# Kernel tuning notes

Measured on AMD Instinct MI355X. Metric: run time of the kernel, lower is better.

The kernel has to match this reference:

```python
import jax, jax.numpy as jnp
import numpy as np

DIM = 256
HEADS = 8
DHEAD = 32
HIDDEN = HEADS * DHEAD
EPS = 1e-5


def layer_norm(x, g, b):
    mu = jnp.mean(x, axis=-1, keepdims=True)
    var = jnp.var(x, axis=-1, keepdims=True)
    return (x - mu) * jax.lax.rsqrt(var + EPS) * g + b


def rope(x):
    # x: [b, m, h, n, d]; interleaved-pair rotary embedding over axis n (lucidrains style)
    n, d = x.shape[-2], x.shape[-1]
    inv_freq = 1.0 / (10000.0 ** (jnp.arange(0, d, 2, dtype=jnp.float32) / d))  # [d/2]
    ang = jnp.arange(n, dtype=jnp.float32)[:, None] * inv_freq[None, :]         # [n, d/2]
    ang = jnp.repeat(ang, 2, axis=-1)                                           # [n, d]
    cos, sin = jnp.cos(ang), jnp.sin(ang)
    xp = x.reshape(x.shape[:-1] + (d // 2, 2))
    rot = jnp.stack((-xp[..., 1], xp[..., 0]), axis=-1).reshape(x.shape)
    return x * cos + rot * sin


def split_heads(t):
    b, m, n, _ = t.shape
    return t.reshape(b, m, n, HEADS, DHEAD).transpose(0, 1, 3, 2, 4)  # b m h n d


def temporal_attention(x, ctx, pos_bias, Wq, Wk, Wv, Wo):
    # x, ctx: [b, m, t, c] (already normalized)
    q = split_heads(x @ Wq) * (DHEAD ** -0.5)
    k = split_heads(ctx @ Wk)
    v = split_heads(ctx @ Wv)
    q, k = rope(q), rope(k)
    sim = jnp.einsum('bmhid,bmhjd->bmhij', q, k) + pos_bias[None]  # pos_bias [1,h,t,t]
    attn = jax.nn.softmax(sim, axis=-1)
    out = jnp.einsum('bmhij,bmhjd->bmhid', attn, v)
    b, m = out.shape[0], out.shape[1]
    out = out.transpose(0, 1, 3, 2, 4).reshape(b, m, -1, HIDDEN)
    return out @ Wo


def setup_inputs() -> dict:
    key = jax.random.key(0)
    ks = jax.random.split(key, 16)
    b, c, t, h, w = 2, DIM, 16, 32, 32
    s = 0.02
    inp = {
        'x': jax.random.normal(ks[0], (b, c, t, h, w), jnp.float32),
        'motion_map': jax.random.normal(ks[1], (b, c, t, h, w), jnp.float32),
        'pos_bias': jax.random.normal(ks[2], (1, HEADS, t, t), jnp.float32),
        'g1': jnp.ones((DIM,), jnp.float32), 'b1': jnp.zeros((DIM,), jnp.float32),
        'Wq1': jax.random.normal(ks[3], (DIM, HIDDEN), jnp.float32) * s,
        'Wk1': jax.random.normal(ks[4], (DIM, HIDDEN), jnp.float32) * s,
        'Wv1': jax.random.normal(ks[5], (DIM, HIDDEN), jnp.float32) * s,
        'Wo1': jax.random.normal(ks[6], (HIDDEN, DIM), jnp.float32) * s,
        'g2': jnp.ones((DIM,), jnp.float32), 'b2': jnp.zeros((DIM,), jnp.float32),
        'cg': jnp.ones((DIM,), jnp.float32), 'cb': jnp.zeros((DIM,), jnp.float32),
        'Wq2': jax.random.normal(ks[7], (DIM, HIDDEN), jnp.float32) * s,
        'Wk2': jax.random.normal(ks[8], (DIM, HIDDEN), jnp.float32) * s,
        'Wv2': jax.random.normal(ks[9], (DIM, HIDDEN), jnp.float32) * s,
        'Wo2': jax.random.normal(ks[10], (HIDDEN, DIM), jnp.float32) * s,
    }
    return inp


def reference(x, motion_map, pos_bias, g1, b1, Wq1, Wk1, Wv1, Wo1,
              g2, b2, cg, cb, Wq2, Wk2, Wv2, Wo2):
    b, c, t, h, w = x.shape
    xs = x.transpose(0, 3, 4, 2, 1).reshape(b, h * w, t, c)           # b (hw) t c
    mm = motion_map.transpose(0, 3, 4, 2, 1).reshape(b, h * w, t, c)
    # self attention
    xn = layer_norm(xs, g1, b1)
    xs = xs + temporal_attention(xn, xn, pos_bias, Wq1, Wk1, Wv1, Wo1)
    # cross attention with motion map
    xn2 = layer_norm(xs, g2, b2)
    ctx = layer_norm(mm, cg, cb)
    xs = xs + temporal_attention(xn2, ctx, pos_bias, Wq2, Wk2, Wv2, Wo2)
    return xs.reshape(b, h, w, t, c).transpose(0, 4, 3, 1, 2)          # b c t h w
```

## Files before the change

kernel.cpp:

```cpp
#include <hip/hip_runtime.h>

typedef __attribute__((ext_vector_type(4))) float f32x4;
typedef __attribute__((ext_vector_type(8))) short s16x8;

__device__ __forceinline__ unsigned short f2bf(float f) {
  union { float f; unsigned int i; } x; x.f = f;
  unsigned int lsb = (x.i >> 16) & 1u;
  x.i += 0x7fffu + lsb;
  return (unsigned short)(x.i >> 16);
}

__device__ __forceinline__ float bf2f(unsigned short u) {
  union { unsigned int i; float f; } x;
  x.i = ((unsigned int)u) << 16;
  return x.f;
}

__device__ __forceinline__ void gload_lds16(const void* gsrc, void* ldst) {
  __builtin_amdgcn_global_load_lds(
      (const __attribute__((address_space(1))) void*)gsrc,
      (__attribute__((address_space(3))) void*)ldst, 16, 0, 0);
}

__global__ void prep_w(const float* __restrict__ Wq1, const float* __restrict__ Wk1,
                       const float* __restrict__ Wv1, const float* __restrict__ Wo1,
                       const float* __restrict__ Wq2, const float* __restrict__ Wk2,
                       const float* __restrict__ Wv2, const float* __restrict__ Wo2,
                       unsigned short* __restrict__ W1t, unsigned short* __restrict__ Wo1t,
                       unsigned short* __restrict__ W2t, unsigned short* __restrict__ Wo2t,
                       float* __restrict__ ropeC, float* __restrict__ ropeS) {
  int blk = blockIdx.x, tid = threadIdx.x;
  if (blk < 768) {
    int n = blk, k = tid;
    const float* src = (n < 256) ? Wq1 : (n < 512 ? Wk1 : Wv1);
    W1t[n * 256 + k] = f2bf(src[k * 256 + (n & 255)]);
  } else if (blk < 1024) {
    int n = blk - 768, k = tid;
    Wo1t[n * 256 + k] = f2bf(Wo1[k * 256 + n]);
  } else if (blk < 1792) {
    int n = blk - 1024, k = tid;
    const float* src = (n < 256) ? Wq2 : (n < 512 ? Wk2 : Wv2);
    W2t[n * 256 + k] = f2bf(src[k * 256 + (n & 255)]);
  } else if (blk < 2048) {
    int n = blk - 1792, k = tid;
    Wo2t[n * 256 + k] = f2bf(Wo2[k * 256 + n]);
  } else {
    #pragma unroll
    for (int it = 0; it < 2; ++it) {
      int idx = it * 256 + tid;
      int t = idx >> 5, d = idx & 31;
      float inv = exp2f(-13.287712379549449f * (float)(d & 30) * (1.0f / 32.0f));
      float ang = (float)t * inv;
      ropeC[idx] = cosf(ang);
      ropeS[idx] = sinf(ang);
    }
  }
}

__global__ __launch_bounds__(256) void transpose_in(
    const float* __restrict__ X, const float* __restrict__ MM,
    void* __restrict__ xtv, void* __restrict__ mmtv, int outBf) {
  __shared__ float lds[32][257];
  int blk = blockIdx.x, tid = threadIdx.x;
  bool isX = blk < 1024;
  int idx = blk & 1023;
  int b = idx >> 9, t = (idx >> 5) & 15, h = idx & 31;
  const float* src = isX ? X : MM;

  int w_ = tid & 31, cg8 = tid >> 5;
  size_t base = (size_t)b * 4194304 + (size_t)t * 1024 + (size_t)h * 32 + w_;
  #pragma unroll
  for (int itr = 0; itr < 32; ++itr) {
    int c = itr * 8 + cg8;
    lds[w_][c] = src[base + (size_t)c * 16384];
  }
  __syncthreads();
  size_t seqb = ((size_t)b * 1024 + (size_t)h * 32) * 16 + t;
  if (outBf) {
    unsigned short* dstp = (unsigned short*)(isX ? xtv : mmtv);
    #pragma unroll
    for (int w2 = 0; w2 < 32; ++w2)
      dstp[(seqb + (size_t)w2 * 16) * 256 + tid] = f2bf(lds[w2][tid]);
  } else {
    float* dstp = (float*)(isX ? xtv : mmtv);
    #pragma unroll
    for (int w2 = 0; w2 < 32; ++w2)
      dstp[(seqb + (size_t)w2 * 16) * 256 + tid] = lds[w2][tid];
  }
}

__global__ __launch_bounds__(256) void ln_rows(
    const void* __restrict__ srcv, const float* __restrict__ gw,
    const float* __restrict__ bw, unsigned short* __restrict__ dst, int srcF32) {
  int tid = threadIdx.x;
  size_t row = (size_t)blockIdx.x * 16 + (tid >> 4);
  int l16 = tid & 15;
  float v[16], s = 0.f, q = 0.f;
  if (srcF32) {
    const float* sp = (const float*)srcv + row * 256 + l16 * 16;
    #pragma unroll
    for (int e = 0; e < 16; ++e) { v[e] = sp[e]; s += v[e]; q += v[e] * v[e]; }
  } else {
    const unsigned short* sp = (const unsigned short*)srcv + row * 256 + l16 * 16;
    #pragma unroll
    for (int e = 0; e < 16; ++e) { v[e] = bf2f(sp[e]); s += v[e]; q += v[e] * v[e]; }
  }
  s += __shfl_xor(s, 1); q += __shfl_xor(q, 1);
  s += __shfl_xor(s, 2); q += __shfl_xor(q, 2);
  s += __shfl_xor(s, 4); q += __shfl_xor(q, 4);
  s += __shfl_xor(s, 8); q += __shfl_xor(q, 8);
  float mu = s * (1.f / 256.f);
  float var = q * (1.f / 256.f) - mu * mu;
  float rs = rsqrtf(fmaxf(var, 0.f) + 1e-5f);
  #pragma unroll
  for (int e = 0; e < 16; ++e) {
    int c = l16 * 16 + e;
    dst[row * 256 + c] = f2bf((v[e] - mu) * rs * gw[c] + bw[c]);
  }
}

__device__ __forceinline__ void stage_tile(const unsigned short* __restrict__ src,
                                           size_t row0, unsigned short* lds,
                                           int k0, int tid) {
  #pragma unroll
  for (int it = 0; it < 2; ++it) {
    int o = (it * 256 + tid) * 16;
    int row = o >> 6;
    int ks = ((o >> 4) & 3) ^ ((row >> 1) & 3);
    gload_lds16(src + (row0 + (size_t)row) * 256 + k0 + ks * 8, (char*)lds + o);
  }
}

__device__ __forceinline__ s16x8 frag_read(const unsigned short* lds, int row, int g) {
  return *(const s16x8*)((const char*)lds + row * 64 + (((g ^ ((row >> 1) & 3)) & 3) << 4));
}

__global__ __launch_bounds__(256) void gemm_qkv(
    const unsigned short* __restrict__ A, const unsigned short* __restrict__ Bt,
    unsigned short* __restrict__ O,
    const float* __restrict__ ropeC, const float* __restrict__ ropeS, int colOff) {
  __shared__ unsigned short lA[2][128 * 32];
  __shared__ unsigned short lB[2][128 * 32];
  __shared__ float lC[512], lS[512];
  int tid = threadIdx.x;
  int m0 = blockIdx.x * 128;
  int n0 = blockIdx.y * 128;
  lC[tid] = ropeC[tid]; lC[tid + 256] = ropeC[tid + 256];
  lS[tid] = ropeS[tid]; lS[tid + 256] = ropeS[tid + 256];

  int lane = tid & 63, wv = tid >> 6;
  int r = lane & 15, g = lane >> 4;
  f32x4 acc[2][8] = {};

  stage_tile(A, m0, lA[0], 0, tid);
  stage_tile(Bt, n0, lB[0], 0, tid);
  __syncthreads();
  for (int ks = 0; ks < 8; ++ks) {
    int cur = ks & 1;
    if (ks < 7) {
      stage_tile(A, m0, lA[cur ^ 1], (ks + 1) * 32, tid);
      stage_tile(Bt, n0, lB[cur ^ 1], (ks + 1) * 32, tid);
    }
    s16x8 af[2], bfr[8];
    #pragma unroll
    for (int mt = 0; mt < 2; ++mt) af[mt] = frag_read(lA[cur], wv * 32 + mt * 16 + r, g);
    #pragma unroll
    for (int nt = 0; nt < 8; ++nt) bfr[nt] = frag_read(lB[cur], nt * 16 + r, g);
    #pragma unroll
    for (int mt = 0; mt < 2; ++mt)
      #pragma unroll
      for (int nt = 0; nt < 8; ++nt)
        acc[mt][nt] = __builtin_amdgcn_mfma_f32_16x16x32_bf16(af[mt], bfr[nt], acc[mt][nt], 0, 0, 0);
    __syncthreads();
  }

  int wrow0 = m0 + wv * 32;
  #pragma unroll
  for (int mt = 0; mt < 2; ++mt) {
    #pragma unroll
    for (int nt = 0; nt < 8; ++nt) {
      int n_g = colOff + n0 + nt * 16 + r;
      int chunk = n_g >> 8;
      f32x4 v = acc[mt][nt];
      int rowb = wrow0 + mt * 16 + 4 * g;
      if (chunk < 2) {
        float scale = (chunk == 0) ? 0.17677669529663687f : 1.0f;
        int d = n_g & 31;
        #pragma unroll
        for (int rr = 0; rr < 4; ++rr) {
          float part = __shfl_xor(v[rr], 1);
          int tt = 4 * g + rr;
          float cc = lC[tt * 32 + d], ss = lS[tt * 32 + d];
          float res = (n_g & 1) ? (v[rr] * cc + part * ss) : (v[rr] * cc - part * ss);
          v[rr] = res * scale;
        }
      }
      #pragma unroll
      for (int rr = 0; rr < 4; ++rr)
        O[(size_t)(rowb + rr) * 768 + n_g] = f2bf(v[rr]);
    }
  }
}

__global__ __launch_bounds__(256) void gemm_out(
    const unsigned short* __restrict__ A, const unsigned short* __restrict__ Bt,
    const unsigned short* __restrict__ resB, const float* __restrict__ resF,
    float* __restrict__ fOut, unsigned short* __restrict__ bOut) {
  __shared__ unsigned short lA[2][128 * 32];
  __shared__ unsigned short lB[2][128 * 32];
  int tid = threadIdx.x;
  int m0 = blockIdx.x * 128;
  int n0 = blockIdx.y * 128;
  int lane = tid & 63, wv = tid >> 6;
  int r = lane & 15, g = lane >> 4;
  f32x4 acc[2][8] = {};

  stage_tile(A, m0, lA[0], 0, tid);
  stage_tile(Bt, n0, lB[0], 0, tid);
  __syncthreads();
  for (int ks = 0; ks < 8; ++ks) {
    int cur = ks & 1;
    if (ks < 7) {
      stage_tile(A, m0, lA[cur ^ 1], (ks + 1) * 32, tid);
      stage_tile(Bt, n0, lB[cur ^ 1], (ks + 1) * 32, tid);
    }
    s16x8 af[2], bfr[8];
    #pragma unroll
    for (int mt = 0; mt < 2; ++mt) af[mt] = frag_read(lA[cur], wv * 32 + mt * 16 + r, g);
    #pragma unroll
    for (int nt = 0; nt < 8; ++nt) bfr[nt] = frag_read(lB[cur], nt * 16 + r, g);
    #pragma unroll
    for (int mt = 0; mt < 2; ++mt)
      #pragma unroll
      for (int nt = 0; nt < 8; ++nt)
        acc[mt][nt] = __builtin_amdgcn_mfma_f32_16x16x32_bf16(af[mt], bfr[nt], acc[mt][nt], 0, 0, 0);
    __syncthreads();
  }

  int wrow0 = m0 + wv * 32;
  #pragma unroll
  for (int mt = 0; mt < 2; ++mt) {
    #pragma unroll
    for (int nt = 0; nt < 8; ++nt) {
      int n_g = n0 + nt * 16 + r;
      int rowb = wrow0 + mt * 16 + 4 * g;
      #pragma unroll
      for (int rr = 0; rr < 4; ++rr) {
        size_t idx = (size_t)(rowb + rr) * 256 + n_g;
        float res = resB ? bf2f(resB[idx]) : resF[idx];
        float val = acc[mt][nt][rr] + res;
        if (fOut) fOut[idx] = val;
        else      bOut[idx] = f2bf(val);
      }
    }
  }
}

__global__ __launch_bounds__(256) void attn_seq(
    const unsigned short* __restrict__ qkvg, const float* __restrict__ pbias,
    unsigned short* __restrict__ aout) {
  __shared__ unsigned short ps[4][2][16][18];
  int tid = threadIdx.x, lane = tid & 63, wv = tid >> 6;
  size_t r0 = (size_t)blockIdx.x * 16;
  int r = lane & 15, g = lane >> 4;

  for (int hs = 0; hs < 2; ++hs) {
    int h = wv * 2 + hs;
    s16x8 kf = *(const s16x8*)&qkvg[(r0 + r) * 768 + 256 + h * 32 + g * 8];
    s16x8 qf = *(const s16x8*)&qkvg[(r0 + r) * 768 +       h * 32 + g * 8];
    f32x4 zero = {};
    f32x4 st = __builtin_amdgcn_mfma_f32_16x16x32_bf16(kf, qf, zero, 0, 0, 0);
    f32x4 bb = *(const f32x4*)&pbias[h * 256 + r * 16 + 4 * g];
    float p0 = st[0] + bb[0], p1 = st[1] + bb[1];
    float p2 = st[2] + bb[2], p3 = st[3] + bb[3];
    float mx = fmaxf(fmaxf(p0, p1), fmaxf(p2, p3));
    mx = fmaxf(mx, __shfl_xor(mx, 16));
    mx = fmaxf(mx, __shfl_xor(mx, 32));
    p0 = __expf(p0 - mx); p1 = __expf(p1 - mx);
    p2 = __expf(p2 - mx); p3 = __expf(p3 - mx);
    float sm = p0 + p1 + p2 + p3;
    sm += __shfl_xor(sm, 16);
    sm += __shfl_xor(sm, 32);
    float inv = 1.0f / sm;
    ps[wv][hs][4 * g + 0][r] = f2bf(p0 * inv);
    ps[wv][hs][4 * g + 1][r] = f2bf(p1 * inv);
    ps[wv][hs][4 * g + 2][r] = f2bf(p2 * inv);
    ps[wv][hs][4 * g + 3][r] = f2bf(p3 * inv);

    #pragma unroll
    for (int dt = 0; dt < 2; ++dt) {
      s16x8 pa, bv;
      #pragma unroll
      for (int e = 0; e < 8; ++e) {
        int j = 8 * g + e;
        int jc = (j < 16) ? j : 0;
        pa[e] = (j < 16) ? (short)ps[wv][hs][jc][r] : (short)0;
        bv[e] = (short)qkvg[(r0 + jc) * 768 + 512 + h * 32 + dt * 16 + r];
      }
      f32x4 o = __builtin_amdgcn_mfma_f32_16x16x32_bf16(pa, bv, zero, 0, 0, 0);
      #pragma unroll
      for (int rr = 0; rr < 4; ++rr)
        aout[(r0 + 4 * g + rr) * 256 + h * 32 + dt * 16 + r] = f2bf(o[rr]);
    }
  }
}

__global__ __launch_bounds__(256) void transpose_out(
    const void* __restrict__ srcv, float* __restrict__ outp, int srcF32) {
  __shared__ float lds[32][257];
  int blk = blockIdx.x, tid = threadIdx.x;
  int b = blk >> 9, t = (blk >> 5) & 15, h = blk & 31;
  size_t seqb = ((size_t)b * 1024 + (size_t)h * 32) * 16 + t;
  if (srcF32) {
    const float* sp = (const float*)srcv;
    #pragma unroll
    for (int w2 = 0; w2 < 32; ++w2)
      lds[w2][tid] = sp[(seqb + (size_t)w2 * 16) * 256 + tid];
  } else {
    const unsigned short* sp = (const unsigned short*)srcv;
    #pragma unroll
    for (int w2 = 0; w2 < 32; ++w2)
      lds[w2][tid] = bf2f(sp[(seqb + (size_t)w2 * 16) * 256 + tid]);
  }
  __syncthreads();
  int w_ = tid & 31, cg8 = tid >> 5;
  size_t base = (size_t)b * 4194304 + (size_t)t * 1024 + (size_t)h * 32 + w_;
  #pragma unroll
  for (int itr = 0; itr < 32; ++itr) {
    int c = itr * 8 + cg8;
    outp[base + (size_t)c * 16384] = lds[w_][c];
  }
}

__global__ __launch_bounds__(256) void fused_stage(
    const float* __restrict__ srcQ, const float* __restrict__ srcK,
    float* __restrict__ dst,
    const float* __restrict__ gq, const float* __restrict__ bq,
    const float* __restrict__ gk, const float* __restrict__ bk,
    const unsigned short* __restrict__ Wqkv, const unsigned short* __restrict__ Wo,
    const float* __restrict__ ropeC, const float* __restrict__ ropeS,
    const float* __restrict__ pbias, int cross) {
  __shared__ unsigned short xnQ[16 * 272];
  __shared__ unsigned short xnK[16 * 272];
  __shared__ unsigned short qkv[16 * 776];
  __shared__ unsigned short ps[4][2][16][18];

  int tid = threadIdx.x, lane = tid & 63, wv = tid >> 6;
  size_t r0 = (size_t)blockIdx.x * 16;
  int r = lane & 15, g = lane >> 4;

  {
    int row = tid >> 4, l16 = tid & 15;
    const float* sp = srcQ + (r0 + row) * 256 + l16 * 16;
    f32x4 v0 = *(const f32x4*)(sp);
    f32x4 v1 = *(const f32x4*)(sp + 4);
    f32x4 v2 = *(const f32x4*)(sp + 8);
    f32x4 v3 = *(const f32x4*)(sp + 12);
    float s = 0.f, q = 0.f;
    #pragma unroll
    for (int e = 0; e < 4; ++e) {
      s += v0[e] + v1[e] + v2[e] + v3[e];
      q += v0[e]*v0[e] + v1[e]*v1[e] + v2[e]*v2[e] + v3[e]*v3[e];
    }
    s += __shfl_xor(s, 1); q += __shfl_xor(q, 1);
    s += __shfl_xor(s, 2); q += __shfl_xor(q, 2);
    s += __shfl_xor(s, 4); q += __shfl_xor(q, 4);
    s += __shfl_xor(s, 8); q += __shfl_xor(q, 8);
    float mu = s * (1.f / 256.f);
    float var = q * (1.f / 256.f) - mu * mu;
    float rs = rsqrtf(fmaxf(var, 0.f) + 1e-5f);
    #pragma unroll
    for (int e = 0; e < 16; ++e) {
      int c = l16 * 16 + e;
      float v = (e < 4) ? v0[e] : (e < 8) ? v1[e - 4] : (e < 12) ? v2[e - 8] : v3[e - 12];
      xnQ[row * 272 + c] = f2bf((v - mu) * rs * gq[c] + bq[c]);
    }
    if (cross) {
      const float* kp = srcK + (r0 + row) * 256 + l16 * 16;
      f32x4 k0 = *(const f32x4*)(kp);
      f32x4 k1 = *(const f32x4*)(kp + 4);
      f32x4 k2 = *(const f32x4*)(kp + 8);
      f32x4 k3 = *(const f32x4*)(kp + 12);
      float sk = 0.f, qk = 0.f;
      #pragma unroll
      for (int e = 0; e < 4; ++e) {
        sk += k0[e] + k1[e] + k2[e] + k3[e];
        qk += k0[e]*k0[e] + k1[e]*k1[e] + k2[e]*k2[e] + k3[e]*k3[e];
      }
      sk += __shfl_xor(sk, 1); qk += __shfl_xor(qk, 1);
      sk += __shfl_xor(sk, 2); qk += __shfl_xor(qk, 2);
      sk += __shfl_xor(sk, 4); qk += __shfl_xor(qk, 4);
      sk += __shfl_xor(sk, 8); qk += __shfl_xor(qk, 8);
      float muk = sk * (1.f / 256.f);
      float vark = qk * (1.f / 256.f) - muk * muk;
      float rsk = rsqrtf(fmaxf(vark, 0.f) + 1e-5f);
      #pragma unroll
      for (int e = 0; e < 16; ++e) {
        int c = l16 * 16 + e;
        float v = (e < 4) ? k0[e] : (e < 8) ? k1[e - 4] : (e < 12) ? k2[e - 8] : k3[e - 12];
        xnK[row * 272 + c] = f2bf((v - muk) * rsk * gk[c] + bk[c]);
      }
    }
  }
  __syncthreads();

  const unsigned short* xnKp = cross ? xnK : xnQ;

  #pragma unroll 2
  for (int it = 0; it < 12; ++it) {
    int n0 = (wv * 12 + it) * 16;
    const unsigned short* xs = (n0 < 256) ? xnQ : xnKp;
    f32x4 acc0 = {}, acc1 = {};
    #pragma unroll
    for (int kc = 0; kc < 4; ++kc) {
      s16x8 af0 = *(const s16x8*)&xs[r * 272 + kc * 32 + g * 8];
      s16x8 bf0 = *(const s16x8*)&Wqkv[(size_t)(n0 + r) * 256 + kc * 32 + g * 8];
      acc0 = __builtin_amdgcn_mfma_f32_16x16x32_bf16(af0, bf0, acc0, 0, 0, 0);
      s16x8 af1 = *(const s16x8*)&xs[r * 272 + (kc + 4) * 32 + g * 8];
      s16x8 bf1 = *(const s16x8*)&Wqkv[(size_t)(n0 + r) * 256 + (kc + 4) * 32 + g * 8];
      acc1 = __builtin_amdgcn_mfma_f32_16x16x32_bf16(af1, bf1, acc1, 0, 0, 0);
    }
    f32x4 acc = acc0 + acc1;
    int n = n0 + r;
    if (n0 < 512) {
      float scale = (n0 < 256) ? 0.17677669529663687f : 1.0f;
      int d = n & 31;
      #pragma unroll
      for (int rr = 0; rr < 4; ++rr) {
        float part = __shfl_xor(acc[rr], 1);
        int tok = 4 * g + rr;
        float cc = ropeC[tok * 32 + d], ss = ropeS[tok * 32 + d];
        float val = (n & 1) ? (acc[rr] * cc + part * ss)
                            : (acc[rr] * cc - part * ss);
        qkv[tok * 776 + n] = f2bf(val * scale);
      }
    } else {
      #pragma unroll
      for (int rr = 0; rr < 4; ++rr)
        qkv[(4 * g + rr) * 776 + n] = f2bf(acc[rr]);
    }
  }
  __syncthreads();

  unsigned short* aout = xnQ;
  for (int hs = 0; hs < 2; ++hs) {
    int h = wv * 2 + hs;
    s16x8 kf = *(const s16x8*)&qkv[r * 776 + 256 + h * 32 + g * 8];
    s16x8 qf = *(const s16x8*)&qkv[r * 776 +       h * 32 + g * 8];
    f32x4 zero = {};
    f32x4 st = __builtin_amdgcn_mfma_f32_16x16x32_bf16(kf, qf, zero, 0, 0, 0);
    f32x4 bb = *(const f32x4*)&pbias[h * 256 + r * 16 + 4 * g];
    float p0 = st[0] + bb[0], p1 = st[1] + bb[1];
    float p2 = st[2] + bb[2], p3 = st[3] + bb[3];
    float mx = fmaxf(fmaxf(p0, p1), fmaxf(p2, p3));
    mx = fmaxf(mx, __shfl_xor(mx, 16));
    mx = fmaxf(mx, __shfl_xor(mx, 32));
    p0 = __expf(p0 - mx); p1 = __expf(p1 - mx);
    p2 = __expf(p2 - mx); p3 = __expf(p3 - mx);
    float sm = p0 + p1 + p2 + p3;
    sm += __shfl_xor(sm, 16);
    sm += __shfl_xor(sm, 32);
    float inv = 1.0f / sm;
    ps[wv][hs][4 * g + 0][r] = f2bf(p0 * inv);
    ps[wv][hs][4 * g + 1][r] = f2bf(p1 * inv);
    ps[wv][hs][4 * g + 2][r] = f2bf(p2 * inv);
    ps[wv][hs][4 * g + 3][r] = f2bf(p3 * inv);

    #pragma unroll
    for (int dt = 0; dt < 2; ++dt) {
      s16x8 pa, bv;
      #pragma unroll
      for (int e = 0; e < 8; ++e) {
        int j = 8 * g + e;
        int jc = (j < 16) ? j : 0;
        pa[e] = (j < 16) ? (short)ps[wv][hs][jc][r] : (short)0;
        bv[e] = (short)qkv[jc * 776 + 512 + h * 32 + dt * 16 + r];
      }
      f32x4 o = __builtin_amdgcn_mfma_f32_16x16x32_bf16(pa, bv, zero, 0, 0, 0);
      #pragma unroll
      for (int rr = 0; rr < 4; ++rr)
        aout[(4 * g + rr) * 272 + h * 32 + dt * 16 + r] = f2bf(o[rr]);
    }
  }
  __syncthreads();

  #pragma unroll 2
  for (int it = 0; it < 4; ++it) {
    int n0 = (wv * 4 + it) * 16;
    f32x4 acc0 = {}, acc1 = {};
    #pragma unroll
    for (int kc = 0; kc < 4; ++kc) {
      s16x8 af0 = *(const s16x8*)&aout[r * 272 + kc * 32 + g * 8];
      s16x8 bf0 = *(const s16x8*)&Wo[(size_t)(n0 + r) * 256 + kc * 32 + g * 8];
      acc0 = __builtin_amdgcn_mfma_f32_16x16x32_bf16(af0, bf0, acc0, 0, 0, 0);
      s16x8 af1 = *(const s16x8*)&aout[r * 272 + (kc + 4) * 32 + g * 8];
      s16x8 bf1 = *(const s16x8*)&Wo[(size_t)(n0 + r) * 256 + (kc + 4) * 32 + g * 8];
      acc1 = __builtin_amdgcn_mfma_f32_16x16x32_bf16(af1, bf1, acc1, 0, 0, 0);
    }
    f32x4 acc = acc0 + acc1;
    #pragma unroll
    for (int rr = 0; rr < 4; ++rr) {
      int tok = 4 * g + rr, n = n0 + r;
      size_t idx = (r0 + tok) * 256 + n;
      dst[idx] = acc[rr] + srcQ[idx];
    }
  }
}

extern "C" void kernel_launch(void* const* d_in, const int* in_sizes, int n_in,
                              void* d_out, int out_size, void* d_ws, size_t ws_size,
                              hipStream_t stream) {
  const float* x   = (const float*)d_in[0];
  const float* mm  = (const float*)d_in[1];
  const float* pb  = (const float*)d_in[2];
  const float* g1  = (const float*)d_in[3];
  const float* b1  = (const float*)d_in[4];
  const float* Wq1 = (const float*)d_in[5];
  const float* Wk1 = (const float*)d_in[6];
  const float* Wv1 = (const float*)d_in[7];
  const float* Wo1 = (const float*)d_in[8];
  const float* g2  = (const float*)d_in[9];
  const float* b2  = (const float*)d_in[10];
  const float* cg  = (const float*)d_in[11];
  const float* cb  = (const float*)d_in[12];
  const float* Wq2 = (const float*)d_in[13];
  const float* Wk2 = (const float*)d_in[14];
  const float* Wv2 = (const float*)d_in[15];
  const float* Wo2 = (const float*)d_in[16];

  char* ws = (char*)d_ws;
  unsigned short* W1t  = (unsigned short*)(ws + 0);
  unsigned short* Wo1t = (unsigned short*)(ws + 393216);
  unsigned short* W2t  = (unsigned short*)(ws + 524288);
  unsigned short* Wo2t = (unsigned short*)(ws + 917504);
  float* ropeC         = (float*)(ws + 1048576);
  float* ropeS         = (float*)(ws + 1050624);

  prep_w<<<2049, 256, 0, stream>>>(Wq1, Wk1, Wv1, Wo1, Wq2, Wk2, Wv2, Wo2,
                                   W1t, Wo1t, W2t, Wo2t, ropeC, ropeS);

  if (ws_size >= 118493184u) {
    unsigned short* xt_bf  = (unsigned short*)(ws + 1052672);
    unsigned short* mmt_bf = (unsigned short*)(ws + 17829888);
    unsigned short* xnA    = (unsigned short*)(ws + 34607104);
    unsigned short* xnB    = (unsigned short*)(ws + 51384320);
    unsigned short* qkv    = (unsigned short*)(ws + 68161536);
    unsigned short* aout   = xnA;
    unsigned short* rows2  = xt_bf;
    float* xs1             = (float*)d_out;
    float* outp            = (float*)d_out;

    transpose_in<<<2048, 256, 0, stream>>>(x, mm, xt_bf, mmt_bf, 1);
    ln_rows<<<2048, 256, 0, stream>>>(xt_bf, g1, b1, xnA, 0);
    ln_rows<<<2048, 256, 0, stream>>>(mmt_bf, cg, cb, xnB, 0);
    gemm_qkv<<<dim3(256, 6), 256, 0, stream>>>(xnA, W1t, qkv, ropeC, ropeS, 0);
    attn_seq<<<2048, 256, 0, stream>>>(qkv, pb, aout);
    gemm_out<<<dim3(256, 2), 256, 0, stream>>>(aout, Wo1t, xt_bf, nullptr, xs1, nullptr);
    ln_rows<<<2048, 256, 0, stream>>>(xs1, g2, b2, xnA, 1);
    gemm_qkv<<<dim3(256, 2), 256, 0, stream>>>(xnA, W2t, qkv, ropeC, ropeS, 0);
    gemm_qkv<<<dim3(256, 4), 256, 0, stream>>>(xnB, W2t + 65536, qkv, ropeC, ropeS, 256);
    attn_seq<<<2048, 256, 0, stream>>>(qkv, pb, aout);
    gemm_out<<<dim3(256, 2), 256, 0, stream>>>(aout, Wo2t, nullptr, xs1, nullptr, rows2);
    transpose_out<<<1024, 256, 0, stream>>>(rows2, outp, 0);
  } else {
    float* xt  = (float*)(ws + 1052672);
    float* mmt = (float*)(ws + 34607104);
    float* xs1 = (float*)d_out;
    float* outp = (float*)d_out;

    transpose_in<<<2048, 256, 0, stream>>>(x, mm, xt, mmt, 0);
    fused_stage<<<2048, 256, 0, stream>>>(xt, xt, xs1, g1, b1, g1, b1,
                                          W1t, Wo1t, ropeC, ropeS, pb, 0);
    fused_stage<<<2048, 256, 0, stream>>>(xs1, mmt, xt, g2, b2, cg, cb,
                                          W2t, Wo2t, ropeC, ropeS, pb, 1);
    transpose_out<<<1024, 256, 0, stream>>>(xt, outp, 1);
  }
}
```

Before: 218.2 us.

## Fuse input LayerNorms into transpose kernel and merge cross-attn QKV GEMMs

```diff
diff --git a/kernel.cpp b/kernel.cpp
--- a/kernel.cpp
+++ b/kernel.cpp
@@ -57,15 +57,20 @@
   }
 }
 
-__global__ __launch_bounds__(256) void transpose_in(
+__global__ __launch_bounds__(256) void transpose_ln(
     const float* __restrict__ X, const float* __restrict__ MM,
-    void* __restrict__ xtv, void* __restrict__ mmtv, int outBf) {
+    const float* __restrict__ g1w, const float* __restrict__ b1w,
+    const float* __restrict__ cgw, const float* __restrict__ cbw,
+    unsigned short* __restrict__ xt_raw, unsigned short* __restrict__ xnA,
+    unsigned short* __restrict__ xnB) {
   __shared__ float lds[32][257];
   int blk = blockIdx.x, tid = threadIdx.x;
   bool isX = blk < 1024;
   int idx = blk & 1023;
   int b = idx >> 9, t = (idx >> 5) & 15, h = idx & 31;
   const float* src = isX ? X : MM;
+  const float* gw  = isX ? g1w : cgw;
+  const float* bw  = isX ? b1w : cbw;
 
   int w_ = tid & 31, cg8 = tid >> 5;
   size_t base = (size_t)b * 4194304 + (size_t)t * 1024 + (size_t)h * 32 + w_;
@@ -75,36 +80,76 @@
     lds[w_][c] = src[base + (size_t)c * 16384];
   }
   __syncthreads();
+
   size_t seqb = ((size_t)b * 1024 + (size_t)h * 32) * 16 + t;
-  if (outBf) {
-    unsigned short* dstp = (unsigned short*)(isX ? xtv : mmtv);
+  if (isX) {
     #pragma unroll
     for (int w2 = 0; w2 < 32; ++w2)
-      dstp[(seqb + (size_t)w2 * 16) * 256 + tid] = f2bf(lds[w2][tid]);
-  } else {
-    float* dstp = (float*)(isX ? xtv : mmtv);
-    #pragma unroll
-    for (int w2 = 0; w2 < 32; ++w2)
-      dstp[(seqb + (size_t)w2 * 16) * 256 + tid] = lds[w2][tid];
-  }
+      xt_raw[(seqb + (size_t)w2 * 16) * 256 + tid] = f2bf(lds[w2][tid]);
+  }
+
+  unsigned short* dst = isX ? xnA : xnB;
+  int l16 = tid & 15;
+  #pragma unroll
+  for (int rr2 = 0; rr2 < 2; ++rr2) {
+    int w = rr2 * 16 + (tid >> 4);
+    float v[16], s = 0.f, q = 0.f;
+    #pragma unroll
+    for (int e = 0; e < 16; ++e) {
+      v[e] = lds[w][l16 * 16 + e];
+      s += v[e]; q += v[e] * v[e];
+    }
+    s += __shfl_xor(s, 1); q += __shfl_xor(q, 1);
+    s += __shfl_xor(s, 2); q += __shfl_xor(q, 2);
+    s += __shfl_xor(s, 4); q += __shfl_xor(q, 4);
+    s += __shfl_xor(s, 8); q += __shfl_xor(q, 8);
+    float mu = s * (1.f / 256.f);
+    float var = q * (1.f / 256.f) - mu * mu;
+    float rs = rsqrtf(fmaxf(var, 0.f) + 1e-5f);
+    size_t orow = (seqb + (size_t)w * 16) * 256;
+    #pragma unroll
+    for (int e = 0; e < 16; ++e) {
+      int c = l16 * 16 + e;
+      dst[orow + c] = f2bf((v[e] - mu) * rs * gw[c] + bw[c]);
+    }
+  }
+}
+
+__global__ __launch_bounds__(256) void transpose_in(
+    const float* __restrict__ X, const float* __restrict__ MM,
+    float* __restrict__ xtv, float* __restrict__ mmtv) {
+  __shared__ float lds[32][257];
+  int blk = blockIdx.x, tid = threadIdx.x;
+  bool isX = blk < 1024;
+  int idx = blk & 1023;
+  int b = idx >> 9, t = (idx >> 5) & 15, h = idx & 31;
+  const float* src = isX ? X : MM;
+  float* dstp = isX ? xtv : mmtv;
+
+  int w_ = tid & 31, cg8 = tid >> 5;
+  size_t base = (size_t)b * 4194304 + (size_t)t * 1024 + (size_t)h * 32 + w_;
+  #pragma unroll
+  for (int itr = 0; itr < 32; ++itr) {
+    int c = itr * 8 + cg8;
+    lds[w_][c] = src[base + (size_t)c * 16384];
+  }
+  __syncthreads();
+  size_t seqb = ((size_t)b * 1024 + (size_t)h * 32) * 16 + t;
+  #pragma unroll
+  for (int w2 = 0; w2 < 32; ++w2)
+    dstp[(seqb + (size_t)w2 * 16) * 256 + tid] = lds[w2][tid];
 }
 
 __global__ __launch_bounds__(256) void ln_rows(
-    const void* __restrict__ srcv, const float* __restrict__ gw,
-    const float* __restrict__ bw, unsigned short* __restrict__ dst, int srcF32) {
+    const float* __restrict__ srcv, const float* __restrict__ gw,
+    const float* __restrict__ bw, unsigned short* __restrict__ dst) {
   int tid = threadIdx.x;
   size_t row = (size_t)blockIdx.x * 16 + (tid >> 4);
   int l16 = tid & 15;
+  const float* sp = srcv + row * 256 + l16 * 16;
   float v[16], s = 0.f, q = 0.f;
-  if (srcF32) {
-    const float* sp = (const float*)srcv + row * 256 + l16 * 16;
-    #pragma unroll
-    for (int e = 0; e < 16; ++e) { v[e] = sp[e]; s += v[e]; q += v[e] * v[e]; }
-  } else {
-    const unsigned short* sp = (const unsigned short*)srcv + row * 256 + l16 * 16;
-    #pragma unroll
-    for (int e = 0; e < 16; ++e) { v[e] = bf2f(sp[e]); s += v[e]; q += v[e] * v[e]; }
-  }
+  #pragma unroll
+  for (int e = 0; e < 16; ++e) { v[e] = sp[e]; s += v[e]; q += v[e] * v[e]; }
   s += __shfl_xor(s, 1); q += __shfl_xor(q, 1);
   s += __shfl_xor(s, 2); q += __shfl_xor(q, 2);
   s += __shfl_xor(s, 4); q += __shfl_xor(q, 4);
@@ -136,15 +181,16 @@
 }
 
 __global__ __launch_bounds__(256) void gemm_qkv(
-    const unsigned short* __restrict__ A, const unsigned short* __restrict__ Bt,
-    unsigned short* __restrict__ O,
-    const float* __restrict__ ropeC, const float* __restrict__ ropeS, int colOff) {
+    const unsigned short* __restrict__ Aq, const unsigned short* __restrict__ Akv,
+    const unsigned short* __restrict__ Bt, unsigned short* __restrict__ O,
+    const float* __restrict__ ropeC, const float* __restrict__ ropeS) {
   __shared__ unsigned short lA[2][128 * 32];
   __shared__ unsigned short lB[2][128 * 32];
   __shared__ float lC[512], lS[512];
   int tid = threadIdx.x;
   int m0 = blockIdx.x * 128;
   int n0 = blockIdx.y * 128;
+  const unsigned short* A = (n0 < 256) ? Aq : Akv;
   lC[tid] = ropeC[tid]; lC[tid + 256] = ropeC[tid + 256];
   lS[tid] = ropeS[tid]; lS[tid + 256] = ropeS[tid + 256];
 
@@ -179,7 +225,7 @@
   for (int mt = 0; mt < 2; ++mt) {
     #pragma unroll
     for (int nt = 0; nt < 8; ++nt) {
-      int n_g = colOff + n0 + nt * 16 + r;
+      int n_g = n0 + nt * 16 + r;
       int chunk = n_g >> 8;
       f32x4 v = acc[mt][nt];
       int rowb = wrow0 + mt * 16 + 4 * g;
@@ -541,7 +587,6 @@
 
   if (ws_size >= 118493184u) {
     unsigned short* xt_bf  = (unsigned short*)(ws + 1052672);
-    unsigned short* mmt_bf = (unsigned short*)(ws + 17829888);
     unsigned short* xnA    = (unsigned short*)(ws + 34607104);
     unsigned short* xnB    = (unsigned short*)(ws + 51384320);
     unsigned short* qkv    = (unsigned short*)(ws + 68161536);
@@ -550,15 +595,12 @@
     float* xs1             = (float*)d_out;
     float* outp            = (float*)d_out;
 
-    transpose_in<<<2048, 256, 0, stream>>>(x, mm, xt_bf, mmt_bf, 1);
-    ln_rows<<<2048, 256, 0, stream>>>(xt_bf, g1, b1, xnA, 0);
-    ln_rows<<<2048, 256, 0, stream>>>(mmt_bf, cg, cb, xnB, 0);
-    gemm_qkv<<<dim3(256, 6), 256, 0, stream>>>(xnA, W1t, qkv, ropeC, ropeS, 0);
+    transpose_ln<<<2048, 256, 0, stream>>>(x, mm, g1, b1, cg, cb, xt_bf, xnA, xnB);
+    gemm_qkv<<<dim3(256, 6), 256, 0, stream>>>(xnA, xnA, W1t, qkv, ropeC, ropeS);
     attn_seq<<<2048, 256, 0, stream>>>(qkv, pb, aout);
     gemm_out<<<dim3(256, 2), 256, 0, stream>>>(aout, Wo1t, xt_bf, nullptr, xs1, nullptr);
-    ln_rows<<<2048, 256, 0, stream>>>(xs1, g2, b2, xnA, 1);
-    gemm_qkv<<<dim3(256, 2), 256, 0, stream>>>(xnA, W2t, qkv, ropeC, ropeS, 0);
-    gemm_qkv<<<dim3(256, 4), 256, 0, stream>>>(xnB, W2t + 65536, qkv, ropeC, ropeS, 256);
+    ln_rows<<<2048, 256, 0, stream>>>(xs1, g2, b2, xnA);
+    gemm_qkv<<<dim3(256, 6), 256, 0, stream>>>(xnA, xnB, W2t, qkv, ropeC, ropeS);
     attn_seq<<<2048, 256, 0, stream>>>(qkv, pb, aout);
     gemm_out<<<dim3(256, 2), 256, 0, stream>>>(aout, Wo2t, nullptr, xs1, nullptr, rows2);
     transpose_out<<<1024, 256, 0, stream>>>(rows2, outp, 0);
@@ -568,7 +610,7 @@
     float* xs1 = (float*)d_out;
     float* outp = (float*)d_out;
 
-    transpose_in<<<2048, 256, 0, stream>>>(x, mm, xt, mmt, 0);
+    transpose_in<<<2048, 256, 0, stream>>>(x, mm, xt, mmt);
     fused_stage<<<2048, 256, 0, stream>>>(xt, xt, xs1, g1, b1, g1, b1,
                                           W1t, Wo1t, ropeC, ropeS, pb, 0);
     fused_stage<<<2048, 256, 0, stream>>>(xs1, mmt, xt, g2, b2, cg, cb,
```

Result: faster. 195.9 us (-10.2%).
